# Kernel optimization log

Hardware: AMD Instinct MI355X
Metric: run time of the kernel (lower is better)

The kernel has to match this reference:

```python
import jax, jax.numpy as jnp
import numpy as np

NEG_SLOPE = 0.01
LN_EPS = 1e-5


def leaky_relu(x):
    return jax.nn.leaky_relu(x, NEG_SLOPE)


def layer_norm(x, w, b):
    mu = jnp.mean(x, axis=-1, keepdims=True)
    var = jnp.var(x, axis=-1, keepdims=True)
    return (x - mu) * jax.lax.rsqrt(var + LN_EPS) * w + b


def setup_inputs() -> dict:
    key = jax.random.key(0)
    B, N, IN_DIM, OUT_DIM = 16, 1024, 512, 512
    ks = jax.random.split(key, 12)
    s_in = 1.0 / np.sqrt(IN_DIM)
    s_n = 1.0 / np.sqrt(N)
    return {
        "node_feats": jax.random.normal(ks[0], (B, N, IN_DIM), jnp.float32),
        "adj_matrix": jax.random.uniform(ks[1], (B, N, N), jnp.float32),
        "linear_w": jax.random.uniform(ks[2], (OUT_DIM, IN_DIM), jnp.float32, -s_in, s_in),
        "linear_b": jax.random.uniform(ks[3], (OUT_DIM,), jnp.float32, -s_in, s_in),
        "q_w": jax.random.uniform(ks[4], (N, N), jnp.float32, -s_n, s_n),
        "q_b": jax.random.uniform(ks[5], (N,), jnp.float32, -s_n, s_n),
        "k_w": jax.random.uniform(ks[6], (N, N), jnp.float32, -s_n, s_n),
        "k_b": jax.random.uniform(ks[7], (N,), jnp.float32, -s_n, s_n),
        "v_w": jax.random.uniform(ks[8], (N, N), jnp.float32, -s_n, s_n),
        "v_b": jax.random.uniform(ks[9], (N,), jnp.float32, -s_n, s_n),
        "norm1_w": jnp.ones((N,), jnp.float32),
        "norm1_b": jnp.zeros((N,), jnp.float32),
        "norm2_w": jnp.ones((OUT_DIM,), jnp.float32),
        "norm2_b": jnp.zeros((OUT_DIM,), jnp.float32),
        "edge_weight": jnp.ones((N, N), jnp.float32),
    }


def reference(node_feats, adj_matrix, linear_w, linear_b, q_w, q_b, k_w, k_b,
              v_w, v_b, norm1_w, norm1_b, norm2_w, norm2_b, edge_weight):
    N = edge_weight.shape[0]
    channel_scale = N ** (-0.5)

    # weighted adjacency + symmetric degree normalization (D^-1/2 A D^-1/2)
    W_A = adj_matrix * jax.nn.sigmoid(edge_weight)          # [B,N,N]
    d_inv_sqrt = jnp.power(jnp.sum(W_A, axis=-1), -0.5)     # [B,N]
    d_inv_sqrt = jnp.where(jnp.isinf(d_inv_sqrt), 0.0, d_inv_sqrt)
    W_A = d_inv_sqrt[:, :, None] * W_A * d_inv_sqrt[:, None, :]

    # node projection + channel-wise self-attention
    X = leaky_relu(jnp.einsum('bni,oi->bno', node_feats, linear_w) + linear_b)  # [B,N,O]
    Tx = jnp.swapaxes(X, -1, -2)                             # [B,O,N]
    Tx = layer_norm(Tx, norm1_w, norm1_b)
    q = jnp.einsum('bxh,gh->bxg', Tx, q_w) + q_b
    k = jnp.einsum('bxh,gh->bxg', Tx, k_w) + k_b
    v = leaky_relu(jnp.einsum('bxh,gh->bxg', Tx, v_w) + v_b)
    att = jax.nn.softmax(jnp.einsum('bxh,byh->bxy', q, k) * channel_scale, axis=-1)
    Tx = Tx + jnp.einsum('bxy,byh->bxh', att, v)

    # graph propagation + final norm
    X = jnp.swapaxes(Tx, -1, -2)                             # [B,N,O]
    X = jnp.einsum('bnm,bmo->bno', W_A, X)
    return layer_norm(X, norm2_w, norm2_b)
```

## Files before the change

### kernel.cpp

```cpp
#include <hip/hip_runtime.h>


typedef __bf16 bf16x8 __attribute__((ext_vector_type(8)));
typedef float  f32x4  __attribute__((ext_vector_type(4)));

#define DEV __device__ __forceinline__

DEV float bf2f(unsigned short u) {
  union { unsigned i; float f; } x; x.i = ((unsigned)u) << 16; return x.f;
}
DEV unsigned short f2bf(float f) {
  unsigned u = __float_as_uint(f);
  u += 0x7fffu + ((u >> 16) & 1u);
  return (unsigned short)(u >> 16);
}
DEV float sigmoidf_(float x) { return 1.0f / (1.0f + __expf(-x)); }

DEV float wave_sum(float v) {
#pragma unroll
  for (int o = 32; o > 0; o >>= 1) v += __shfl_xor(v, o, 64);
  return v;
}
DEV float wave_max(float v) {
#pragma unroll
  for (int o = 32; o > 0; o >>= 1) v = fmaxf(v, __shfl_xor(v, o, 64));
  return v;
}

DEV void gload16(const unsigned short* g, unsigned short* l) {
  __builtin_amdgcn_global_load_lds(
      (const __attribute__((address_space(1))) unsigned int*)g,
      (__attribute__((address_space(3))) unsigned int*)l, 16, 0, 0);
}

#define BARD()       asm volatile("s_waitcnt lgkmcnt(0)\n\ts_barrier" ::: "memory")
#define WAIT_VM(n)   asm volatile("s_waitcnt vmcnt(" #n ")" ::: "memory")

__global__ __launch_bounds__(256) void cast5_kernel(
    const float* __restrict__ s0, unsigned short* __restrict__ d0,
    const float* __restrict__ s1, unsigned short* __restrict__ d1,
    const float* __restrict__ s2, unsigned short* __restrict__ d2,
    const float* __restrict__ s3, unsigned short* __restrict__ d3,
    const float* __restrict__ s4, unsigned short* __restrict__ d4) {
  const int c0 = 2097152;
  const int c1 = c0 + 65536;
  const int c2 = c1 + 262144;
  const int c3 = c2 + 262144;
  int g = blockIdx.x * 256 + threadIdx.x;
  const float* s; unsigned short* d; int i;
  if (g < c0)      { s = s0; d = d0; i = g; }
  else if (g < c1) { s = s1; d = d1; i = g - c0; }
  else if (g < c2) { s = s2; d = d2; i = g - c1; }
  else if (g < c3) { s = s3; d = d3; i = g - c2; }
  else             { s = s4; d = d4; i = g - c3; }
  float4 v = *(const float4*)(s + (size_t)i * 4);
  ushort4 o;
  o.x = f2bf(v.x); o.y = f2bf(v.y); o.z = f2bf(v.z); o.w = f2bf(v.w);
  *(ushort4*)(d + (size_t)i * 4) = o;
}

__global__ __launch_bounds__(256) void sigrow_kernel(const float* __restrict__ adj,
                                                     const float* __restrict__ edge,
                                                     float* __restrict__ dis) {
  __shared__ float sh[4];
  size_t row = blockIdx.x;
  int n = (int)(row & 1023);
  const float* ar = adj + row * 1024;
  const float* er = edge + (size_t)n * 1024;
  int c = threadIdx.x * 4;
  float4 a4 = *(const float4*)(ar + c);
  float4 e4 = *(const float4*)(er + c);
  float s = a4.x * sigmoidf_(e4.x) + a4.y * sigmoidf_(e4.y) +
            a4.z * sigmoidf_(e4.z) + a4.w * sigmoidf_(e4.w);
  s = wave_sum(s);
  if ((threadIdx.x & 63) == 0) sh[threadIdx.x >> 6] = s;
  __syncthreads();
  if (threadIdx.x == 0) {
    float t = sh[0] + sh[1] + sh[2] + sh[3];
    dis[row] = t > 0.0f ? rsqrtf(t) : 0.0f;
  }
}

__global__ __launch_bounds__(256) void wa_kernel(const float* __restrict__ adj,
                                                 const float* __restrict__ edge,
                                                 const float* __restrict__ dis,
                                                 unsigned short* __restrict__ wa) {
  size_t g = (size_t)blockIdx.x * 256 + threadIdx.x;
  int m = (int)(g & 255) * 4;
  size_t rest = g >> 8;
  int n = (int)(rest & 1023);
  int b = (int)(rest >> 10);
  float4 a4 = *(const float4*)(adj + rest * 1024 + m);
  float4 e4 = *(const float4*)(edge + (size_t)n * 1024 + m);
  float dn = dis[rest];
  float4 dm = *(const float4*)(dis + (size_t)b * 1024 + m);
  ushort4 o;
  o.x = f2bf(dn * a4.x * sigmoidf_(e4.x) * dm.x);
  o.y = f2bf(dn * a4.y * sigmoidf_(e4.y) * dm.y);
  o.z = f2bf(dn * a4.z * sigmoidf_(e4.z) * dm.z);
  o.w = f2bf(dn * a4.w * sigmoidf_(e4.w) * dm.w);
  *(ushort4*)(wa + g * 4) = o;
}

template <int VPT, int NW, bool OUTF32>
__global__ void ln_kernel(const unsigned short* __restrict__ in,
                          const float* __restrict__ gw,
                          const float* __restrict__ gb,
                          void* __restrict__ out, int D) {
  __shared__ float sh[2 * NW];
  size_t row = blockIdx.x;
  const unsigned short* x = in + row * (size_t)D;
  int base = threadIdx.x * VPT;
  float v[VPT];
  ushort4 u = *(const ushort4*)(x + base);
  v[0] = bf2f(u.x); v[1] = bf2f(u.y); v[2] = bf2f(u.z); v[3] = bf2f(u.w);
  float s = 0.f, sq = 0.f;
#pragma unroll
  for (int i = 0; i < VPT; i++) { s += v[i]; sq += v[i] * v[i]; }
  s = wave_sum(s); sq = wave_sum(sq);
  int wv = threadIdx.x >> 6;
  if ((threadIdx.x & 63) == 0) { sh[wv] = s; sh[NW + wv] = sq; }
  __syncthreads();
  s = 0.f; sq = 0.f;
#pragma unroll
  for (int i = 0; i < NW; i++) { s += sh[i]; sq += sh[NW + i]; }
  float mean = s / D;
  float var = sq / D - mean * mean;
  float rs = rsqrtf(fmaxf(var, 0.0f) + 1e-5f);
#pragma unroll
  for (int i = 0; i < VPT; i++) {
    float y = (v[i] - mean) * rs * gw[base + i] + gb[base + i];
    if (OUTF32) ((float*)out)[row * D + base + i] = y;
    else        ((unsigned short*)out)[row * D + base + i] = f2bf(y);
  }
}

__global__ __launch_bounds__(256) void softmax_kernel(const float* __restrict__ in,
                                                      const float* __restrict__ in2,
                                                      unsigned short* __restrict__ out) {
  __shared__ float sh[4];
  size_t row = blockIdx.x;
  const float* x = in + row * 512;
  const float* x2 = in2 + row * 512;
  float2 u = *(const float2*)(x + threadIdx.x * 2);
  float2 u2 = *(const float2*)(x2 + threadIdx.x * 2);
  float a = (u.x + u2.x) * 0.03125f, b = (u.y + u2.y) * 0.03125f;
  float m = wave_max(fmaxf(a, b));
  int wid = threadIdx.x >> 6;
  if ((threadIdx.x & 63) == 0) sh[wid] = m;
  __syncthreads();
  m = fmaxf(fmaxf(sh[0], sh[1]), fmaxf(sh[2], sh[3]));
  __syncthreads();
  float e0 = __expf(a - m), e1 = __expf(b - m);
  float s = wave_sum(e0 + e1);
  if ((threadIdx.x & 63) == 0) sh[wid] = s;
  __syncthreads();
  s = sh[0] + sh[1] + sh[2] + sh[3];
  float inv = 1.0f / s;
  ushort2 o; o.x = f2bf(e0 * inv); o.y = f2bf(e1 * inv);
  *(ushort2*)(out + row * 512 + threadIdx.x * 2) = o;
}

#define MFMA16(d, s0, s1) d = __builtin_amdgcn_mfma_f32_16x16x32_bf16(s0, s1, d, 0, 0, 0)

#define STGA(bi, kt) do { \
  _Pragma("unroll") for (int h = 0; h < 4; h++) \
    gload16(gA + (size_t)(h * 32) * Kr + (size_t)(kt) * 64, \
            As + (bi) * 8192 + h * 2048 + ldst); \
} while (0)
#define STGB(bi, kt) do { \
  _Pragma("unroll") for (int h = 0; h < 4; h++) \
    gload16(gB + (size_t)(h * 32) * Kr + (size_t)(kt) * 64, \
            Bs + (bi) * 8192 + h * 2048 + ldst); \
} while (0)

#define LDA(bi) do { \
  _Pragma("unroll") for (int mf = 0; mf < 4; mf++) { \
    a[mf][0] = *(const bf16x8*)&As[(bi) * 8192 + arow + mf * 1024 + xs0]; \
    a[mf][1] = *(const bf16x8*)&As[(bi) * 8192 + arow + mf * 1024 + xs1]; \
  } } while (0)
#define LDB(bi) do { \
  _Pragma("unroll") for (int nf = 0; nf < 4; nf++) { \
    bb[nf][0] = *(const bf16x8*)&Bs[(bi) * 8192 + brow + nf * 1024 + xs0]; \
    bb[nf][1] = *(const bf16x8*)&Bs[(bi) * 8192 + brow + nf * 1024 + xs1]; \
  } } while (0)

#define MMALL() do { \
  _Pragma("unroll") for (int mf = 0; mf < 4; mf++) \
  _Pragma("unroll") for (int nf = 0; nf < 4; nf++) { \
    MFMA16(acc[mf][nf], a[mf][0], bb[nf][0]); \
    MFMA16(acc[mf][nf], a[mf][1], bb[nf][1]); \
  } } while (0)

#define TILE1(P, kt, SG) do { \
  WAIT_VM(0); \
  BARD(); \
  if (SG) { STGA((P) ^ 1, (kt) + 1); STGB((P) ^ 1, (kt) + 1); } \
  LDA(P); LDB(P); \
  MMALL(); \
} while (0)

template <int BIAS , bool LEAKY, bool RESID,
          bool OUTF32, bool SPLIT, bool SPLITK>
__global__ __launch_bounds__(256, 2) void gemm128(
    const unsigned short* __restrict__ A, size_t sA,
    const unsigned short* __restrict__ Bt, size_t sB,
    const float* __restrict__ bias, const float* __restrict__ bias2,
    const unsigned short* __restrict__ resid,
    void* __restrict__ out, void* __restrict__ out2,
    int M, int NcS, int K, int Kst, int lgx, int lgy, int xh) {
  __shared__ unsigned short As[2 * 8192];
  __shared__ unsigned short Bs[2 * 8192];
  const int qc = gridDim.x >> 3;
  const int dd = blockIdx.x;
  const int lb = (dd & 7) * qc + (dd >> 3);
  const int x = lb & ((1 << lgx) - 1);
  const int y = (lb >> lgx) & ((1 << lgy) - 1);
  const int b = (lb >> (lgx + lgy)) & 15;
  const int sk = SPLITK ? (lb >> (lgx + lgy + 4)) : 0;

  const int tid = threadIdx.x;
  const int wid = tid >> 6, lane = tid & 63;
  const int wr = wid >> 1, wc = wid & 1;
  const int l15 = lane & 15, l4 = lane >> 4;
  const int tM = y * 128, tN = x * 128;
  const size_t Kr = (size_t)Kst;

  const int srow = wid * 8 + (lane >> 3);
  const int scol = ((lane & 7) ^ ((lane >> 3) & 7)) * 8;
  const int koff = sk * K;
  const unsigned short* gA = A + sA * b + (size_t)(tM + srow) * Kr + scol + koff;
  const unsigned short* gB = Bt + sB * b + (size_t)(tN + srow) * Kr + scol + koff;
  const int ldst = wid * 512;

  const int xs0 = ((0 * 4 + l4) ^ (lane & 7)) * 8;
  const int xs1 = ((1 * 4 + l4) ^ (lane & 7)) * 8;
  const int arow = (wr * 64 + l15) * 64;
  const int brow = (wc * 64 + l15) * 64;

  f32x4 acc[4][4] = {};
  bf16x8 a[4][2], bb[4][2];

  const int nt = K >> 6;
  STGA(0, 0); STGB(0, 0);

  for (int kt = 0; kt < nt; ++kt)
    TILE1(kt & 1, kt, kt < nt - 1);

  const float* bia = bias;
  void* o = out;
  if (SPLIT && x >= xh) { bia = bias2; o = out2; }
  if (SPLITK && sk) o = out2;
  const size_t ob = (size_t)M * NcS * b;
#pragma unroll
  for (int mf = 0; mf < 4; mf++)
#pragma unroll
    for (int nf = 0; nf < 4; nf++) {
      const int cg = tN + wc * 64 + nf * 16 + l15;
      const int rbase = tM + wr * 64 + mf * 16 + l4 * 4;
#pragma unroll
      for (int r = 0; r < 4; r++) {
        const int rg = rbase + r;
        float v = acc[mf][nf][r];
        if (BIAS == 1) v += bia[rg];
        if (BIAS == 2) v += bia[cg];
        if (LEAKY) v = v > 0.0f ? v : 0.01f * v;
        const size_t idx = ob + (size_t)rg * NcS + cg;
        if (RESID) v += bf2f(resid[idx]);
        if (OUTF32) ((float*)o)[idx] = v;
        else        ((unsigned short*)o)[idx] = f2bf(v);
      }
    }
}

extern "C" void kernel_launch(void* const* d_in, const int* in_sizes, int n_in,
                              void* d_out, int out_size, void* d_ws, size_t ws_size,
                              hipStream_t stream) {
  const float* node_feats = (const float*)d_in[0];
  const float* adj        = (const float*)d_in[1];
  const float* linear_w   = (const float*)d_in[2];
  const float* linear_b   = (const float*)d_in[3];
  const float* q_w        = (const float*)d_in[4];
  const float* q_b        = (const float*)d_in[5];
  const float* k_w        = (const float*)d_in[6];
  const float* k_b        = (const float*)d_in[7];
  const float* v_w        = (const float*)d_in[8];
  const float* v_b        = (const float*)d_in[9];
  const float* n1w        = (const float*)d_in[10];
  const float* n1b        = (const float*)d_in[11];
  const float* n2w        = (const float*)d_in[12];
  const float* n2b        = (const float*)d_in[13];
  const float* edge       = (const float*)d_in[14];
  float* out = (float*)d_out;

  const int B = 16, N = 1024, C = 512;
  const size_t MiB = 1u << 20;
  char* w = (char*)d_ws;
  unsigned short* nf_bf   = (unsigned short*)(w);
  unsigned short* Xt_bf   = (unsigned short*)(w + 16 * MiB);
  float*          att_raw = (float*)(w);
  float*          att_raw2= (float*)(w + 16 * MiB);
  unsigned short* WA_bf   = (unsigned short*)(w);
  unsigned short* Txln    = (unsigned short*)(w + 32 * MiB);
  unsigned short* q_bf    = (unsigned short*)(w + 48 * MiB);
  unsigned short* X3_bf   = (unsigned short*)(w + 48 * MiB);
  unsigned short* k_bf    = (unsigned short*)(w + 64 * MiB);
  unsigned short* att_bf  = (unsigned short*)(w + 64 * MiB);
  unsigned short* vt_bf   = (unsigned short*)(w + 80 * MiB);
  unsigned short* Tx2_bf  = (unsigned short*)(w + 96 * MiB);
  unsigned short* lw_bf   = (unsigned short*)(w + 112 * MiB);
  unsigned short* qw_bf   = (unsigned short*)(w + 113 * MiB);
  unsigned short* kw_bf   = (unsigned short*)(w + 115 * MiB);
  unsigned short* vw_bf   = (unsigned short*)(w + 117 * MiB);
  float*          dis     = (float*)(w + 119 * MiB);

  cast5_kernel<<<(2949120 + 255) / 256, 256, 0, stream>>>(
      node_feats, nf_bf, linear_w, lw_bf, q_w, qw_bf, k_w, kw_bf, v_w, vw_bf);

  sigrow_kernel<<<B * N, 256, 0, stream>>>(adj, edge, dis);

  gemm128<1, true, false, false, false, false><<<512, 256, 0, stream>>>(
      lw_bf, 0, nf_bf, (size_t)N * C, linear_b, nullptr, nullptr,
      Xt_bf, nullptr, C, N, C, C, 3, 2, 999);

  ln_kernel<4, 4, false><<<B * C, 256, 0, stream>>>(Xt_bf, n1w, n1b, Txln, N);

  gemm128<2, false, false, false, true, false><<<1024, 256, 0, stream>>>(
      Txln, (size_t)C * N, qw_bf, 0, q_b, k_b - 1024, nullptr,
      q_bf, (void*)(k_bf - 1024), C, N, N, N, 4, 2, 8);

  gemm128<1, true, false, false, false, false><<<512, 256, 0, stream>>>(
      vw_bf, 0, Txln, (size_t)C * N, v_b, nullptr, nullptr,
      vt_bf, nullptr, N, C, N, N, 2, 3, 999);

  gemm128<0, false, false, true, false, true><<<512, 256, 0, stream>>>(
      q_bf, (size_t)C * N, k_bf, (size_t)C * N, nullptr, nullptr, nullptr,
      att_raw, att_raw2, C, C, 512, N, 2, 2, 999);

  softmax_kernel<<<B * C, 256, 0, stream>>>(att_raw, att_raw2, att_bf);

  wa_kernel<<<B * N * N / 4 / 256, 256, 0, stream>>>(adj, edge, dis, WA_bf);

  gemm128<0, false, true, false, false, false><<<512, 256, 0, stream>>>(
      att_bf, (size_t)C * C, vt_bf, (size_t)N * C, nullptr, nullptr, Txln,
      Tx2_bf, nullptr, C, N, C, C, 3, 2, 999);

  gemm128<0, false, false, false, false, false><<<512, 256, 0, stream>>>(
      WA_bf, (size_t)N * N, Tx2_bf, (size_t)C * N, nullptr, nullptr, nullptr,
      X3_bf, nullptr, N, C, N, N, 2, 3, 999);

  ln_kernel<4, 2, true><<<B * N, 128, 0, stream>>>(X3_bf, n2w, n2b, out, C);
}
```

Baseline: 202.0 us.

## Switch GEMM to triple-buffered K=32 tiles with deeper prefetch

```diff
diff --git a/kernel.cpp b/kernel.cpp
--- a/kernel.cpp
+++ b/kernel.cpp
@@ -163,54 +163,39 @@
 
 #define MFMA16(d, s0, s1) d = __builtin_amdgcn_mfma_f32_16x16x32_bf16(s0, s1, d, 0, 0, 0)
 
-#define STGA(bi, kt) do { \
-  _Pragma("unroll") for (int h = 0; h < 4; h++) \
-    gload16(gA + (size_t)(h * 32) * Kr + (size_t)(kt) * 64, \
-            As + (bi) * 8192 + h * 2048 + ldst); \
+#define STG(bo, kt) do { \
+  gload16(gA + (size_t)(kt) * 32, As + (bo) + ldst); \
+  gload16(gA + rowskip + (size_t)(kt) * 32, As + (bo) + 2048 + ldst); \
+  gload16(gB + (size_t)(kt) * 32, Bs + (bo) + ldst); \
+  gload16(gB + rowskip + (size_t)(kt) * 32, Bs + (bo) + 2048 + ldst); \
 } while (0)
-#define STGB(bi, kt) do { \
-  _Pragma("unroll") for (int h = 0; h < 4; h++) \
-    gload16(gB + (size_t)(h * 32) * Kr + (size_t)(kt) * 64, \
-            Bs + (bi) * 8192 + h * 2048 + ldst); \
+
+#define LDA(bo) do { \
+  _Pragma("unroll") for (int mf = 0; mf < 4; mf++) \
+    a[mf] = *(const bf16x8*)&As[(bo) + (wr * 64 + mf * 16 + l15) * 32 + xsw]; \
 } while (0)
-
-#define LDA(bi) do { \
-  _Pragma("unroll") for (int mf = 0; mf < 4; mf++) { \
-    a[mf][0] = *(const bf16x8*)&As[(bi) * 8192 + arow + mf * 1024 + xs0]; \
-    a[mf][1] = *(const bf16x8*)&As[(bi) * 8192 + arow + mf * 1024 + xs1]; \
-  } } while (0)
-#define LDB(bi) do { \
-  _Pragma("unroll") for (int nf = 0; nf < 4; nf++) { \
-    bb[nf][0] = *(const bf16x8*)&Bs[(bi) * 8192 + brow + nf * 1024 + xs0]; \
-    bb[nf][1] = *(const bf16x8*)&Bs[(bi) * 8192 + brow + nf * 1024 + xs1]; \
-  } } while (0)
+#define LDB(bo) do { \
+  _Pragma("unroll") for (int nf = 0; nf < 4; nf++) \
+    bb[nf] = *(const bf16x8*)&Bs[(bo) + (wc * 64 + nf * 16 + l15) * 32 + xsw]; \
+} while (0)
 
 #define MMALL() do { \
   _Pragma("unroll") for (int mf = 0; mf < 4; mf++) \
-  _Pragma("unroll") for (int nf = 0; nf < 4; nf++) { \
-    MFMA16(acc[mf][nf], a[mf][0], bb[nf][0]); \
-    MFMA16(acc[mf][nf], a[mf][1], bb[nf][1]); \
-  } } while (0)
-
-#define TILE1(P, kt, SG) do { \
-  WAIT_VM(0); \
-  BARD(); \
-  if (SG) { STGA((P) ^ 1, (kt) + 1); STGB((P) ^ 1, (kt) + 1); } \
-  LDA(P); LDB(P); \
-  MMALL(); \
+  _Pragma("unroll") for (int nf = 0; nf < 4; nf++) \
+    MFMA16(acc[mf][nf], a[mf], bb[nf]); \
 } while (0)
 
 template <int BIAS , bool LEAKY, bool RESID,
           bool OUTF32, bool SPLIT, bool SPLITK>
-__global__ __launch_bounds__(256, 2) void gemm128(
+__global__ __launch_bounds__(256) void gemm128(
     const unsigned short* __restrict__ A, size_t sA,
     const unsigned short* __restrict__ Bt, size_t sB,
     const float* __restrict__ bias, const float* __restrict__ bias2,
     const unsigned short* __restrict__ resid,
     void* __restrict__ out, void* __restrict__ out2,
     int M, int NcS, int K, int Kst, int lgx, int lgy, int xh) {
-  __shared__ unsigned short As[2 * 8192];
-  __shared__ unsigned short Bs[2 * 8192];
+  __shared__ unsigned short As[3 * 4096];
+  __shared__ unsigned short Bs[3 * 4096];
   const int qc = gridDim.x >> 3;
   const int dd = blockIdx.x;
   const int lb = (dd & 7) * qc + (dd >> 3);
@@ -226,26 +211,31 @@
   const int tM = y * 128, tN = x * 128;
   const size_t Kr = (size_t)Kst;
 
-  const int srow = wid * 8 + (lane >> 3);
-  const int scol = ((lane & 7) ^ ((lane >> 3) & 7)) * 8;
+  const int srow = wid * 16 + (lane >> 2);
+  const int scol = ((lane & 3) ^ ((lane >> 3) & 3)) * 8;
   const int koff = sk * K;
   const unsigned short* gA = A + sA * b + (size_t)(tM + srow) * Kr + scol + koff;
   const unsigned short* gB = Bt + sB * b + (size_t)(tN + srow) * Kr + scol + koff;
+  const size_t rowskip = (size_t)64 * Kr;
   const int ldst = wid * 512;
 
-  const int xs0 = ((0 * 4 + l4) ^ (lane & 7)) * 8;
-  const int xs1 = ((1 * 4 + l4) ^ (lane & 7)) * 8;
-  const int arow = (wr * 64 + l15) * 64;
-  const int brow = (wc * 64 + l15) * 64;
-
+  const int xsw = ((l4 ^ ((l15 >> 1) & 3)) * 8);
   f32x4 acc[4][4] = {};
-  bf16x8 a[4][2], bb[4][2];
-
-  const int nt = K >> 6;
-  STGA(0, 0); STGB(0, 0);
-
-  for (int kt = 0; kt < nt; ++kt)
-    TILE1(kt & 1, kt, kt < nt - 1);
+  bf16x8 a[4], bb[4];
+
+  const int nt = K >> 5;
+  STG(0, 0);
+  STG(4096, 1);
+  int p0 = 0, p1 = 4096, p2 = 8192;
+
+  for (int kt = 0; kt < nt; ++kt) {
+    if (kt == nt - 1) { WAIT_VM(0); } else { WAIT_VM(4); }
+    BARD();
+    if (kt < nt - 2) STG(p2, kt + 2);
+    LDA(p0); LDB(p0);
+    MMALL();
+    int tmp = p0; p0 = p1; p1 = p2; p2 = tmp;
+  }
 
   const float* bia = bias;
   void* o = out;
```

Measured after the change: 228.7 us. 1.13x slower.
